# Optimization experiments

Measured on AMD Instinct MI355X. Metric: run time of the kernel, lower is better.

Reference implementation:

```python
import jax, jax.numpy as jnp
import numpy as np
from jax import lax

T, B, E, H, L = 256, 128, 512, 1024, 2


def setup_inputs() -> dict:
    key = jax.random.key(0)
    ks = jax.random.split(key, 12)
    x = jax.random.normal(ks[0], (T, B, E), dtype=jnp.float32)
    # PackedSequence batch_sizes: descending, first == max batch
    bs = jnp.sort(jax.random.randint(ks[1], (T,), 1, B + 1).astype(jnp.int32))[::-1]
    bs = bs.at[0].set(B)
    unsorted_indices = jax.random.permutation(ks[2], B).astype(jnp.int32)
    s = 1.0 / np.sqrt(H)
    def u(k, shape):
        return jax.random.uniform(k, shape, jnp.float32, -s, s)
    return {
        "x": x,
        "W_ih0": u(ks[3], (3 * H, E)), "W_hh0": u(ks[4], (3 * H, H)),
        "b_ih0": u(ks[5], (3 * H,)), "b_hh0": u(ks[6], (3 * H,)),
        "W_ih1": u(ks[7], (3 * H, H)), "W_hh1": u(ks[8], (3 * H, H)),
        "b_ih1": u(ks[9], (3 * H,)), "b_hh1": u(ks[10], (3 * H,)),
        "batch_sizes": bs,
        "unsorted_indices": unsorted_indices,
    }


def gru_cell(x, h, W_ih, W_hh, b_ih, b_hh):
    gi = x @ W_ih.T + b_ih          # [b, 3H]
    gh = h @ W_hh.T + b_hh          # [b, 3H]
    i_r, i_z, i_n = jnp.split(gi, 3, axis=-1)
    h_r, h_z, h_n = jnp.split(gh, 3, axis=-1)
    r = jax.nn.sigmoid(i_r + h_r)
    z = jax.nn.sigmoid(i_z + h_z)
    n = jnp.tanh(i_n + r * h_n)
    return (1.0 - z) * n + z * h


def reference(x, W_ih0, W_hh0, b_ih0, b_hh0, W_ih1, W_hh1, b_ih1, b_hh1,
              batch_sizes, unsorted_indices):
    params = [(W_ih0, W_hh0, b_ih0, b_hh0), (W_ih1, W_hh1, b_ih1, b_hh1)]
    row = jnp.arange(B)

    def step(h, inp):
        xt, bs = inp                       # xt: [B, E]
        mask = (row < bs)[:, None]         # active rows this timestep
        layer_in = xt
        new_h = []
        for i in range(L):
            hn = gru_cell(layer_in, h[i], *params[i])
            # inactive rows keep their previous hidden state (packed-seq semantics)
            new_h.append(jnp.where(mask, hn, h[i]))
            layer_in = hn
        return jnp.stack(new_h), None

    h0 = jnp.zeros((L, B, H), dtype=x.dtype)
    h_final, _ = lax.scan(step, h0, (x, batch_sizes))
    # index_select(h, 1, unsorted_indices)
    return h_final[:, unsorted_indices, :]
```

## Files before the change

kernel.cpp:

```cpp
#include <hip/hip_runtime.h>
#include <cstdint>
#include <cstddef>

#define T_ 256
#define B_ 128
#define E_ 512
#define H_ 1024
#define BH (B_*H_)
#define GI (B_*3072)
#define NWG 256

typedef _Float16 v8h __attribute__((ext_vector_type(8)));
typedef float    v4f __attribute__((ext_vector_type(4)));
typedef unsigned int u32x4 __attribute__((ext_vector_type(4)));

__device__ __forceinline__ float sigmoidf_(float x) {
    return 1.0f / (1.0f + __expf(-x));
}
__device__ __forceinline__ float tanhf_(float x) {
    return 1.0f - 2.0f / (__expf(2.0f * x) + 1.0f);
}

__device__ __forceinline__ void sc_store2(void* p, unsigned v) {
    asm volatile("global_store_short %0, %1, off sc0 sc1" :: "v"(p), "v"(v) : "memory");
}
__device__ __forceinline__ void sc_store4(void* p, float v) {
    asm volatile("global_store_dword %0, %1, off sc0 sc1" :: "v"(p), "v"(v) : "memory");
}

__global__ __launch_bounds__(256, 1) void gru_persist(
    const int* __restrict__ bs,
    const _Float16* __restrict__ x16,
    const _Float16* __restrict__ Wi0,
    const _Float16* __restrict__ Wh0,
    const _Float16* __restrict__ Wi1,
    const _Float16* __restrict__ Wh1,
    const float* __restrict__ bias,
    float* __restrict__ h0f, float* __restrict__ h1f,
    _Float16* __restrict__ h0h, _Float16* __restrict__ h1h,
    _Float16* __restrict__ hn0,
    float* __restrict__ gi0, float* __restrict__ gi1,
    int* __restrict__ barctr)
{
    __shared__ _Float16 WL[16 * 48 * 72];
    __shared__ _Float16 AS[2][128][72];

    const int bid = blockIdx.x;
    const int grp = bid >> 6;
    const int sl  = bid & 63;
    const int tid = threadIdx.x;
    const int lane = tid & 63, w = tid >> 6;
    const int m = lane & 15, q = lane >> 4;

    {
        const _Float16* Wsrc; int K;
        if      (grp == 0) { Wsrc = Wi0; K = 512;  }
        else if (grp == 1) { Wsrc = Wh0; K = 1024; }
        else if (grp == 2) { Wsrc = Wi1; K = 1024; }
        else               { Wsrc = Wh1; K = 1024; }
        const bool isAB = (grp & 1);
        const int nchw = K / 64;
        for (int u = tid; u < nchw * 384; u += 256) {
            int kc = u / 384, rem = u % 384, c = rem >> 3, slot = rem & 7;
            int gr = isAB ? ((c >> 4) * 1024 + sl * 16 + (c & 15)) : (sl * 48 + c);
            *(u32x4*)&WL[(kc * 48 + c) * 72 + slot * 8] =
                *(const u32x4*)(Wsrc + (size_t)gr * K + kc * 64 + slot * 8);
        }
    }
    __syncthreads();

    const int colG = sl * 16 + m;
    float br = 0.f, bz = 0.f, bi = 0.f, bh = 0.f;
    if (grp & 1) {
        const float* bb = bias + (grp == 3 ? 4 * H_ : 0);
        br = bb[colG]; bz = bb[H_ + colG];
        bi = bb[2 * H_ + colG]; bh = bb[3 * H_ + colG];
    }

    const int srow = tid >> 1, spart = tid & 1;

    int* shard  = barctr + (bid & 7) * 256;
    int* master = barctr + 8 * 256;
    int* epoch  = barctr + 9 * 256;

    v4f acc[6];

    for (int k = 0; k < T_ + 3; ++k) {
        int t = k - grp + (grp == 0 ? 0 : (grp == 2 ? 0 : 0));
        t = (grp == 0) ? k : (grp == 1) ? k - 1 : (grp == 2) ? k - 2 : k - 3;
        const bool active = (t >= 0) && (t < T_);

        if (active) {
            const int pb = t & 1;
            const int rb = pb ^ 1;
            const _Float16* Abase; int ap, nch;
            if      (grp == 0) { Abase = x16 + (size_t)t * B_ * E_;  ap = E_; nch = 8;  }
            else if (grp == 1) { Abase = h0h + (size_t)rb * BH;      ap = H_; nch = 16; }
            else if (grp == 2) { Abase = hn0 + (size_t)pb * BH;      ap = H_; nch = 16; }
            else               { Abase = h1h + (size_t)rb * BH;      ap = H_; nch = 16; }

#pragma unroll
            for (int i = 0; i < 6; ++i) acc[i] = (v4f){0.f, 0.f, 0.f, 0.f};

            const _Float16* sp = Abase + (size_t)srow * ap + spart * 32;
            u32x4 rv0, rv1, rv2, rv3;
            rv0 = *(const u32x4*)(sp + 0);
            rv1 = *(const u32x4*)(sp + 8);
            rv2 = *(const u32x4*)(sp + 16);
            rv3 = *(const u32x4*)(sp + 24);
            {
                _Float16* d = &AS[0][srow][spart * 32];
                *(u32x4*)(d + 0) = rv0; *(u32x4*)(d + 8)  = rv1;
                *(u32x4*)(d + 16) = rv2; *(u32x4*)(d + 24) = rv3;
            }
            __syncthreads();

            int buf = 0;
            for (int kc = 0; kc < nch; ++kc) {
                const bool more = (kc + 1 < nch);
                if (more) {
                    const _Float16* p = sp + (kc + 1) * 64;
                    rv0 = *(const u32x4*)(p + 0);
                    rv1 = *(const u32x4*)(p + 8);
                    rv2 = *(const u32x4*)(p + 16);
                    rv3 = *(const u32x4*)(p + 24);
                }
                const _Float16* wch = &WL[kc * 48 * 72];
#pragma unroll
                for (int s = 0; s < 2; ++s) {
                    const int ko = s * 32 + q * 8;
                    v8h a0 = *(const v8h*)&AS[buf][32 * w + m][ko];
                    v8h a1 = *(const v8h*)&AS[buf][32 * w + 16 + m][ko];
#pragma unroll
                    for (int g = 0; g < 3; ++g) {
                        v8h b = *(const v8h*)&wch[(g * 16 + m) * 72 + ko];
                        acc[g * 2 + 0] = __builtin_amdgcn_mfma_f32_16x16x32_f16(a0, b, acc[g * 2 + 0], 0, 0, 0);
                        acc[g * 2 + 1] = __builtin_amdgcn_mfma_f32_16x16x32_f16(a1, b, acc[g * 2 + 1], 0, 0, 0);
                    }
                }
                if (more) {
                    _Float16* d = &AS[buf ^ 1][srow][spart * 32];
                    *(u32x4*)(d + 0) = rv0; *(u32x4*)(d + 8)  = rv1;
                    *(u32x4*)(d + 16) = rv2; *(u32x4*)(d + 24) = rv3;
                }
                __syncthreads();
                buf ^= 1;
            }

            if (grp == 0 || grp == 2) {
                float* gw = (grp == 0 ? gi0 : gi1) + (size_t)pb * GI;
                const int cbase = sl * 48;
#pragma unroll
                for (int cf = 0; cf < 3; ++cf)
#pragma unroll
                    for (int rf = 0; rf < 2; ++rf)
#pragma unroll
                        for (int r = 0; r < 4; ++r) {
                            int row = 32 * w + rf * 16 + q * 4 + r;
                            sc_store4(gw + (size_t)row * 3072 + cbase + cf * 16 + m,
                                      acc[cf * 2 + rf][r]);
                        }
            } else {
                const int bs_t = bs[t];
                const float* gr_ = (grp == 1 ? gi0 : gi1) + (size_t)pb * GI;
                float*      hf   = (grp == 1 ? h0f : h1f);
                _Float16*   hh_w = (grp == 1 ? h0h : h1h) + (size_t)pb * BH;
                _Float16*   hn0w = hn0 + (size_t)pb * BH;
#pragma unroll
                for (int rf = 0; rf < 2; ++rf)
#pragma unroll
                    for (int r = 0; r < 4; ++r) {
                        int row = 32 * w + rf * 16 + q * 4 + r;
                        size_t go = (size_t)row * 3072 + colG;
                        float gir = gr_[go];
                        float giz = gr_[go + 1024];
                        float gin = gr_[go + 2048];
                        size_t off = (size_t)row * H_ + colG;
                        float hprev = hf[off];
                        float rr = sigmoidf_(gir + acc[0 + rf][r] + br);
                        float zz = sigmoidf_(giz + acc[2 + rf][r] + bz);
                        float nn = tanhf_(gin + bi + rr * (acc[4 + rf][r] + bh));
                        float hnew = (1.0f - zz) * nn + zz * hprev;
                        bool act = row < bs_t;
                        float hsel = act ? hnew : hprev;
                        if (grp == 1)
                            sc_store2(hn0w + off, (unsigned)__builtin_bit_cast(unsigned short, (_Float16)hnew));
                        sc_store2(hh_w + off, (unsigned)__builtin_bit_cast(unsigned short, (_Float16)hsel));
                        if (act) hf[off] = hnew;
                    }
            }
        }

        if (k < T_ + 2) {
            __syncthreads();
            if (tid == 0) {
                int old = __hip_atomic_fetch_add(shard, 1, __ATOMIC_RELAXED, __HIP_MEMORY_SCOPE_AGENT);
                if (old + 1 == 32 * (k + 1)) {
                    int mo = __hip_atomic_fetch_add(master, 1, __ATOMIC_RELAXED, __HIP_MEMORY_SCOPE_AGENT);
                    if (mo + 1 == 8 * (k + 1))
                        __hip_atomic_store(epoch, k + 1, __ATOMIC_RELEASE, __HIP_MEMORY_SCOPE_AGENT);
                }
                while (__hip_atomic_load(epoch, __ATOMIC_RELAXED, __HIP_MEMORY_SCOPE_AGENT) < k + 1)
                    __builtin_amdgcn_s_sleep(2);
                (void)__hip_atomic_load(epoch, __ATOMIC_ACQUIRE, __HIP_MEMORY_SCOPE_AGENT);
            }
            __syncthreads();
        }
    }
}

__global__ void cvt_f32_f16(const float* __restrict__ s, _Float16* __restrict__ d, int n) {
    int i = (blockIdx.x * 256 + threadIdx.x) * 8;
    if (i >= n) return;
    float4 v0 = *(const float4*)(s + i);
    float4 v1 = *(const float4*)(s + i + 4);
    v8h o = { (_Float16)v0.x, (_Float16)v0.y, (_Float16)v0.z, (_Float16)v0.w,
              (_Float16)v1.x, (_Float16)v1.y, (_Float16)v1.z, (_Float16)v1.w };
    *(v8h*)(d + i) = o;
}

__global__ void prep_bias(const float* __restrict__ bi0, const float* __restrict__ bh0,
                          const float* __restrict__ bi1, const float* __restrict__ bh1,
                          float* __restrict__ bias) {
    int tid = blockIdx.x * 256 + threadIdx.x;
    int l = tid >> 10, j = tid & 1023;
    const float* bi = l ? bi1 : bi0;
    const float* bh = l ? bh1 : bh0;
    float* o = bias + l * 4 * H_;
    o[j]           = bi[j] + bh[j];
    o[H_ + j]      = bi[H_ + j] + bh[H_ + j];
    o[2 * H_ + j]  = bi[2 * H_ + j];
    o[3 * H_ + j]  = bh[2 * H_ + j];
}

__global__ void gather_out(const float* __restrict__ h0f, const float* __restrict__ h1f,
                           const int* __restrict__ unsorted, float* __restrict__ out) {
    int rowid = blockIdx.x;
    int l = rowid >> 7, b = rowid & 127;
    int src = unsorted[b];
    const float* s = (l ? h1f : h0f) + (size_t)src * H_;
    float* o = out + (size_t)rowid * H_;
    int c = threadIdx.x * 4;
    *(float4*)(o + c) = *(const float4*)(s + c);
}

extern "C" void kernel_launch(void* const* d_in, const int* in_sizes, int n_in,
                              void* d_out, int out_size, void* d_ws, size_t ws_size,
                              hipStream_t stream) {
    const float* x    = (const float*)d_in[0];
    const float* Wi0f = (const float*)d_in[1];
    const float* Wh0f = (const float*)d_in[2];
    const float* bi0  = (const float*)d_in[3];
    const float* bh0  = (const float*)d_in[4];
    const float* Wi1f = (const float*)d_in[5];
    const float* Wh1f = (const float*)d_in[6];
    const float* bi1  = (const float*)d_in[7];
    const float* bh1  = (const float*)d_in[8];
    const int*  bs       = (const int*)d_in[9];
    const int*  unsorted = (const int*)d_in[10];
    float* out = (float*)d_out;

    char* ws = (char*)d_ws;
    size_t off = 0;
    auto alloc = [&](size_t bytes) -> char* {
        char* p = ws + off;
        off += (bytes + 255) & ~(size_t)255;
        return p;
    };
    _Float16* x16 = (_Float16*)alloc((size_t)T_ * B_ * E_ * 2);
    _Float16* Wi0 = (_Float16*)alloc((size_t)3 * H_ * E_ * 2);
    _Float16* Wh0 = (_Float16*)alloc((size_t)3 * H_ * H_ * 2);
    _Float16* Wi1 = (_Float16*)alloc((size_t)3 * H_ * H_ * 2);
    _Float16* Wh1 = (_Float16*)alloc((size_t)3 * H_ * H_ * 2);
    float*    bias = (float*)alloc(2 * 4 * H_ * 4);
    float*    gi0  = (float*)alloc((size_t)2 * GI * 4);
    float*    gi1  = (float*)alloc((size_t)2 * GI * 4);
    char* zbase = ws + off;
    float*    h0f = (float*)alloc((size_t)BH * 4);
    float*    h1f = (float*)alloc((size_t)BH * 4);
    _Float16* h0h = (_Float16*)alloc((size_t)2 * BH * 2);
    _Float16* h1h = (_Float16*)alloc((size_t)2 * BH * 2);
    _Float16* hn0 = (_Float16*)alloc((size_t)2 * BH * 2);
    int*      barctr = (int*)alloc(16 * 1024);
    size_t zbytes = (size_t)((ws + off) - zbase);

    (void)hipMemsetAsync(zbase, 0, zbytes, stream);

    cvt_f32_f16<<<(T_ * B_ * E_) / 2048, 256, 0, stream>>>(x, x16, T_ * B_ * E_);
    cvt_f32_f16<<<(3 * H_ * E_) / 2048, 256, 0, stream>>>(Wi0f, Wi0, 3 * H_ * E_);
    cvt_f32_f16<<<(3 * H_ * H_) / 2048, 256, 0, stream>>>(Wh0f, Wh0, 3 * H_ * H_);
    cvt_f32_f16<<<(3 * H_ * H_) / 2048, 256, 0, stream>>>(Wi1f, Wi1, 3 * H_ * H_);
    cvt_f32_f16<<<(3 * H_ * H_) / 2048, 256, 0, stream>>>(Wh1f, Wh1, 3 * H_ * H_);
    prep_bias<<<8, 256, 0, stream>>>(bi0, bh0, bi1, bh1, bias);

    gru_persist<<<256, 256, 0, stream>>>(bs, x16, Wi0, Wh0, Wi1, Wh1, bias,
                                         h0f, h1f, h0h, h1h, hn0, gi0, gi1, barctr);
    gather_out<<<256, 256, 0, stream>>>(h0f, h1f, unsorted, out);
}
```

Before: 5.885 ms.

## Deepen A-tile global prefetch to four chunks and keep fp32 hidden state in registers

The K loop now issues global loads for the A operand four chunks ahead, rotating through four register sets, instead of one chunk ahead. The aim is to hide global/L2 latency behind the MFMA work on each step. The fp32 previous hidden state is kept in per-thread registers across timesteps and written to global memory only once after the loop, which removes a global read and a conditional write per element per step. In exchange register pressure rises (16 extra u32x4), which may lower occupancy or cause spills, and the fp32 hidden buffers are no longer zeroed by the memset.

```diff
diff --git a/kernel.cpp b/kernel.cpp
--- a/kernel.cpp
+++ b/kernel.cpp
@@ -8,7 +8,6 @@
 #define H_ 1024
 #define BH (B_*H_)
 #define GI (B_*3072)
-#define NWG 256
 
 typedef _Float16 v8h __attribute__((ext_vector_type(8)));
 typedef float    v4f __attribute__((ext_vector_type(4)));
@@ -77,6 +76,12 @@
         bi = bb[2 * H_ + colG]; bh = bb[3 * H_ + colG];
     }
 
+    float hm[2][4];
+#pragma unroll
+    for (int rf = 0; rf < 2; ++rf)
+#pragma unroll
+        for (int r = 0; r < 4; ++r) hm[rf][r] = 0.f;
+
     const int srow = tid >> 1, spart = tid & 1;
 
     int* shard  = barctr + (bid & 7) * 256;
@@ -84,10 +89,43 @@
     int* epoch  = barctr + 9 * 256;
 
     v4f acc[6];
+    u32x4 QA0, QA1, QA2, QA3, QB0, QB1, QB2, QB3;
+    u32x4 QC0, QC1, QC2, QC3, QD0, QD1, QD2, QD3;
+
+#define ISSUE(Qv, kcn) do { \
+        const _Float16* p_ = sp + (size_t)(kcn) * 64; \
+        Qv##0 = *(const u32x4*)(p_ + 0);  Qv##1 = *(const u32x4*)(p_ + 8); \
+        Qv##2 = *(const u32x4*)(p_ + 16); Qv##3 = *(const u32x4*)(p_ + 24); \
+    } while (0)
+#define WRITEQ(Qv, dbuf) do { \
+        _Float16* d_ = &AS[dbuf][srow][spart * 32]; \
+        *(u32x4*)(d_ + 0) = Qv##0;  *(u32x4*)(d_ + 8)  = Qv##1; \
+        *(u32x4*)(d_ + 16) = Qv##2; *(u32x4*)(d_ + 24) = Qv##3; \
+    } while (0)
+#define COMPUTE(BUF, KC) do { \
+        const _Float16* wch_ = &WL[(KC) * 48 * 72]; \
+        _Pragma("unroll") \
+        for (int s = 0; s < 2; ++s) { \
+            const int ko = s * 32 + q * 8; \
+            v8h a0 = *(const v8h*)&AS[BUF][32 * w + m][ko]; \
+            v8h a1 = *(const v8h*)&AS[BUF][32 * w + 16 + m][ko]; \
+            _Pragma("unroll") \
+            for (int g = 0; g < 3; ++g) { \
+                v8h b = *(const v8h*)&wch_[(g * 16 + m) * 72 + ko]; \
+                acc[g * 2 + 0] = __builtin_amdgcn_mfma_f32_16x16x32_f16(a0, b, acc[g * 2 + 0], 0, 0, 0); \
+                acc[g * 2 + 1] = __builtin_amdgcn_mfma_f32_16x16x32_f16(a1, b, acc[g * 2 + 1], 0, 0, 0); \
+            } \
+        } \
+    } while (0)
+#define CHUNK_BODY(KC, QI, QW, BUF) do { \
+        if ((KC) + 4 < nch) ISSUE(QI, (KC) + 4); \
+        COMPUTE(BUF, KC); \
+        if ((KC) + 1 < nch) WRITEQ(QW, (BUF) ^ 1); \
+        __syncthreads(); \
+    } while (0)
 
     for (int k = 0; k < T_ + 3; ++k) {
-        int t = k - grp + (grp == 0 ? 0 : (grp == 2 ? 0 : 0));
-        t = (grp == 0) ? k : (grp == 1) ? k - 1 : (grp == 2) ? k - 2 : k - 3;
+        const int t = (grp == 0) ? k : (grp == 1) ? k - 1 : (grp == 2) ? k - 2 : k - 3;
         const bool active = (t >= 0) && (t < T_);
 
         if (active) {
@@ -103,48 +141,16 @@
             for (int i = 0; i < 6; ++i) acc[i] = (v4f){0.f, 0.f, 0.f, 0.f};
 
             const _Float16* sp = Abase + (size_t)srow * ap + spart * 32;
-            u32x4 rv0, rv1, rv2, rv3;
-            rv0 = *(const u32x4*)(sp + 0);
-            rv1 = *(const u32x4*)(sp + 8);
-            rv2 = *(const u32x4*)(sp + 16);
-            rv3 = *(const u32x4*)(sp + 24);
-            {
-                _Float16* d = &AS[0][srow][spart * 32];
-                *(u32x4*)(d + 0) = rv0; *(u32x4*)(d + 8)  = rv1;
-                *(u32x4*)(d + 16) = rv2; *(u32x4*)(d + 24) = rv3;
-            }
+
+            ISSUE(QA, 0); ISSUE(QB, 1); ISSUE(QC, 2); ISSUE(QD, 3);
+            WRITEQ(QA, 0);
             __syncthreads();
 
-            int buf = 0;
-            for (int kc = 0; kc < nch; ++kc) {
-                const bool more = (kc + 1 < nch);
-                if (more) {
-                    const _Float16* p = sp + (kc + 1) * 64;
-                    rv0 = *(const u32x4*)(p + 0);
-                    rv1 = *(const u32x4*)(p + 8);
-                    rv2 = *(const u32x4*)(p + 16);
-                    rv3 = *(const u32x4*)(p + 24);
-                }
-                const _Float16* wch = &WL[kc * 48 * 72];
-#pragma unroll
-                for (int s = 0; s < 2; ++s) {
-                    const int ko = s * 32 + q * 8;
-                    v8h a0 = *(const v8h*)&AS[buf][32 * w + m][ko];
-                    v8h a1 = *(const v8h*)&AS[buf][32 * w + 16 + m][ko];
-#pragma unroll
-                    for (int g = 0; g < 3; ++g) {
-                        v8h b = *(const v8h*)&wch[(g * 16 + m) * 72 + ko];
-                        acc[g * 2 + 0] = __builtin_amdgcn_mfma_f32_16x16x32_f16(a0, b, acc[g * 2 + 0], 0, 0, 0);
-                        acc[g * 2 + 1] = __builtin_amdgcn_mfma_f32_16x16x32_f16(a1, b, acc[g * 2 + 1], 0, 0, 0);
-                    }
-                }
-                if (more) {
-                    _Float16* d = &AS[buf ^ 1][srow][spart * 32];
-                    *(u32x4*)(d + 0) = rv0; *(u32x4*)(d + 8)  = rv1;
-                    *(u32x4*)(d + 16) = rv2; *(u32x4*)(d + 24) = rv3;
-                }
-                __syncthreads();
-                buf ^= 1;
+            for (int base = 0; base < nch; base += 4) {
+                CHUNK_BODY(base + 0, QA, QB, 0);
+                CHUNK_BODY(base + 1, QB, QC, 1);
+                CHUNK_BODY(base + 2, QC, QD, 0);
+                CHUNK_BODY(base + 3, QD, QA, 1);
             }
 
             if (grp == 0 || grp == 2) {
@@ -163,7 +169,6 @@
             } else {
                 const int bs_t = bs[t];
                 const float* gr_ = (grp == 1 ? gi0 : gi1) + (size_t)pb * GI;
-                float*      hf   = (grp == 1 ? h0f : h1f);
                 _Float16*   hh_w = (grp == 1 ? h0h : h1h) + (size_t)pb * BH;
                 _Float16*   hn0w = hn0 + (size_t)pb * BH;
 #pragma unroll
@@ -176,7 +181,7 @@
                         float giz = gr_[go + 1024];
                         float gin = gr_[go + 2048];
                         size_t off = (size_t)row * H_ + colG;
-                        float hprev = hf[off];
+                        float hprev = hm[rf][r];
                         float rr = sigmoidf_(gir + acc[0 + rf][r] + br);
                         float zz = sigmoidf_(giz + acc[2 + rf][r] + bz);
                         float nn = tanhf_(gin + bi + rr * (acc[4 + rf][r] + bh));
@@ -186,7 +191,7 @@
                         if (grp == 1)
                             sc_store2(hn0w + off, (unsigned)__builtin_bit_cast(unsigned short, (_Float16)hnew));
                         sc_store2(hh_w + off, (unsigned)__builtin_bit_cast(unsigned short, (_Float16)hsel));
-                        if (act) hf[off] = hnew;
+                        hm[rf][r] = hsel;
                     }
             }
         }
@@ -207,6 +212,21 @@
             __syncthreads();
         }
     }
+
+    if (grp & 1) {
+        float* hf = (grp == 1) ? h0f : h1f;
+#pragma unroll
+        for (int rf = 0; rf < 2; ++rf)
+#pragma unroll
+            for (int r = 0; r < 4; ++r) {
+                int row = 32 * w + rf * 16 + q * 4 + r;
+                hf[(size_t)row * H_ + colG] = hm[rf][r];
+            }
+    }
+#undef ISSUE
+#undef WRITEQ
+#undef COMPUTE
+#undef CHUNK_BODY
 }
 
 __global__ void cvt_f32_f16(const float* __restrict__ s, _Float16* __restrict__ d, int n) {
@@ -275,9 +295,9 @@
     float*    bias = (float*)alloc(2 * 4 * H_ * 4);
     float*    gi0  = (float*)alloc((size_t)2 * GI * 4);
     float*    gi1  = (float*)alloc((size_t)2 * GI * 4);
+    float*    h0f  = (float*)alloc((size_t)BH * 4);
+    float*    h1f  = (float*)alloc((size_t)BH * 4);
     char* zbase = ws + off;
-    float*    h0f = (float*)alloc((size_t)BH * 4);
-    float*    h1f = (float*)alloc((size_t)BH * 4);
     _Float16* h0h = (_Float16*)alloc((size_t)2 * BH * 2);
     _Float16* h1h = (_Float16*)alloc((size_t)2 * BH * 2);
     _Float16* hn0 = (_Float16*)alloc((size_t)2 * BH * 2);
```

New measurement: 4.855 ms. 1.21x faster.
